# Kernel tuning notes

Hardware: AMD Instinct MI355X
Metric: run time of the kernel (lower is better)

Reference implementation:

```python
import jax, jax.numpy as jnp
import numpy as np


def _cell_centered_coords(H, W):
    # cell-centered unit grid: coordinate k -> (k + 0.5) / n, meshgrid over (h1, w1, h2, w2)
    h = (jnp.arange(H, dtype=jnp.float32) + 0.5) / H
    w = (jnp.arange(W, dtype=jnp.float32) + 0.5) / W
    g = jnp.meshgrid(h, w, h, w, indexing='ij')
    return jnp.stack(g, axis=-1)  # (H, W, H, W, 4)


def setup_inputs() -> dict:
    key = jax.random.key(0)
    ks = jax.random.split(key, 6)
    B, I, O, H, W, HID = 8, 16, 16, 28, 28, 64
    s1 = 1.0 / np.sqrt(4.0)
    s2 = 1.0 / np.sqrt(HID)
    return {
        'v': jax.random.normal(ks[0], (B, I, H, W), dtype=jnp.float32),
        'W1': jax.random.uniform(ks[1], (4, HID), jnp.float32, -s1, s1),
        'b1': jax.random.uniform(ks[2], (HID,), jnp.float32, -s1, s1),
        'W2': jax.random.uniform(ks[3], (HID, O * I), jnp.float32, -s2, s2),
        'b2': jax.random.uniform(ks[4], (O * I,), jnp.float32, -s2, s2),
        'bias': jax.random.uniform(ks[5], (O, 1, 1), jnp.float32, -1.0 / np.sqrt(I), 1.0 / np.sqrt(I)),
    }


def reference(v, W1, b1, W2, b2, bias):
    H, W = v.shape[-2], v.shape[-1]
    I = v.shape[-3]
    O = W2.shape[-1] // I
    coords = _cell_centered_coords(H, W)                      # (H,W,H,W,4)
    hidden = jax.nn.gelu(coords @ W1 + b1, approximate=False)  # (H,W,H,W,64)
    kernel = (hidden @ W2 + b2).reshape(H, W, H, W, O, I)      # (h1,w1,h2,w2,O,I)
    # midpoint-rule quadrature weights on the unit square: 1/(H*W) per cell
    quad = 1.0 / (H * W)
    # einsum 'h1 w1 h2 w2 o i, n i h1 w2 -> n o h2 w2' (w1 summed out of kernel alone)
    out = jnp.einsum('pqrsoi,nips->nors', kernel, quad * v)
    return out + bias
```

## Files before the change

kernel.cpp:

```cpp
#include <hip/hip_runtime.h>

#define Hn 28
#define PQ 784
#define NI 128

typedef __attribute__((ext_vector_type(8))) short short8v;
typedef __attribute__((ext_vector_type(4))) float float4v;

__device__ __forceinline__ short f2bf(float x) {
    union { float f; unsigned u; } a; a.f = x;
    unsigned r = a.u + 0x7FFF + ((a.u >> 16) & 1);
    return (short)(r >> 16);
}

__global__ __launch_bounds__(256) void prep_kernel(
    const float* __restrict__ v, const float* __restrict__ W2,
    short* __restrict__ vTb, short* __restrict__ W2b, float* __restrict__ Vsum)
{
    const int b = blockIdx.x;
    const int t = threadIdx.x;
    if (b == NI) {
        for (int e = t; e < 8192; e += 256) {
            const float2 f = ((const float2*)W2)[e];
            short2 h; h.x = f2bf(f.x); h.y = f2bf(f.y);
            ((short2*)W2b)[e] = h;
        }
        return;
    }
    const int ni = b;
    for (int e = t; e < PQ; e += 256) {
        const int p = e / Hn;
        const int s = e - p * Hn;
        vTb[s * (NI * 32) + ni * 32 + p] = f2bf(v[ni * PQ + e]);
    }
    if (t < Hn) {
        *(uint2*)(vTb + t * (NI * 32) + ni * 32 + 28) = make_uint2(0u, 0u);
    }
    if (t < Hn) {
        const int s = t;
        float acc = 0.0f;
        #pragma unroll
        for (int p = 0; p < Hn; ++p) acc += v[ni * PQ + p * Hn + s];
        Vsum[s * NI + ni] = acc;
    }
}

__global__ __launch_bounds__(256, 4) void fused_kernel(
    const short* __restrict__ vTb, const short* __restrict__ W2b,
    const float* __restrict__ Vsum,
    const float* __restrict__ W1, const float* __restrict__ b1,
    const float* __restrict__ b2, const float* __restrict__ bias,
    float* __restrict__ out)
{
    __shared__ short sV[NI * 40];
    __shared__ short sHt[64 * 40];
    __shared__ short sTa[8 * 1032];
    __shared__ float sRed[4 * 256];
    __shared__ float sVs[NI];

    const int t = threadIdx.x;
    const int rs = blockIdx.x;
    const int r = rs / Hn;
    const int s = rs - r * Hn;

    {
        const short* src = vTb + s * (NI * 32);
        #pragma unroll
        for (int j = 0; j < 2; ++j) {
            const int idx = t + 256 * j;
            const int ni = idx >> 2;
            const int ko = (idx & 3) * 8;
            *(short8v*)&sV[ni * 40 + ko] = *(const short8v*)(src + ni * 32 + ko);
        }
    }
    if (t < NI) sVs[t] = Vsum[s * NI + t];

    {
        const int c = t & 63;
        const int pg = t >> 6;
        const float w0 = W1[c];
        const float Wc = W1[64 + c];
        const float w2 = W1[128 + c];
        const float w3 = W1[192 + c];
        const float inv = 1.0f / 28.0f;
        const float base = ((r + 0.5f) * inv) * w2 + ((s + 0.5f) * inv) * w3
                         + b1[c] + 0.5f * Wc;
        const float w0i = inv * w0;
        const float W2c = Wc * Wc;
        const float c2 = 1.1651786f * W2c;
        const float c4 = 0.0145213f * (W2c * W2c);
        #pragma unroll
        for (int pi = 0; pi < 7; ++pi) {
            const int p = pg * 7 + pi;
            const float m  = fmaf((float)p + 0.5f, w0i, base);
            const float m2 = m * m;
            const float E  = __builtin_amdgcn_exp2f(m2 * -0.72134752f);
            const float az = fabsf(m) * 0.70710678f;
            const float tt = __builtin_amdgcn_rcpf(fmaf(0.3275911f, az, 1.0f));
            float poly = fmaf(tt, 1.061405429f, -1.453152027f);
            poly = fmaf(tt, poly, 1.421413741f);
            poly = fmaf(tt, poly, -0.284496736f);
            poly = fmaf(tt, poly, 0.254829592f);
            poly = poly * tt;
            float erfv = fmaf(-poly, E, 1.0f);
            erfv = (m < 0.0f) ? -erfv : erfv;
            const float g   = 0.5f * m * (1.0f + erfv);
            const float phi = 0.39894228f * E;
            const float p4  = fmaf(-m2, m2, fmaf(7.0f, m2, -4.0f));
            const float corr = phi * fmaf(c4, p4, c2 * (2.0f - m2));
            sHt[c * 40 + p] = f2bf(fmaf(28.0f, g, corr));
        }
        if (pg == 3) *(uint2*)&sHt[c * 40 + 28] = make_uint2(0u, 0u);
    }
    __syncthreads();

    const int w  = t >> 6;
    const int l  = t & 63;
    const int lm = l & 15;
    const int q  = l >> 4;
    const int k0 = q * 8;

    {
        short8v aF[2], bF[4];
        aF[0] = *(const short8v*)&sV[(32 * w + lm) * 40 + k0];
        aF[1] = *(const short8v*)&sV[(32 * w + 16 + lm) * 40 + k0];
        #pragma unroll
        for (int nt = 0; nt < 4; ++nt)
            bF[nt] = *(const short8v*)&sHt[(16 * nt + lm) * 40 + k0];

        float4v accD[2][4];
        #pragma unroll
        for (int mt = 0; mt < 2; ++mt)
            #pragma unroll
            for (int nt = 0; nt < 4; ++nt)
                accD[mt][nt] = __builtin_amdgcn_mfma_f32_16x16x32_bf16(
                    aF[mt], bF[nt], (float4v)(0.0f), 0, 0, 0);

        #pragma unroll
        for (int mt = 0; mt < 2; ++mt) {
            const int n8 = 2 * w + mt;
            #pragma unroll
            for (int nt = 0; nt < 4; ++nt) {
                const int c = 16 * nt + lm;
                #pragma unroll
                for (int reg = 0; reg < 4; ++reg) {
                    const int i = q * 4 + reg;
                    sTa[n8 * 1032 + c * 16 + i] = f2bf(accD[mt][nt][reg]);
                }
            }
        }
    }
    __syncthreads();

    float4v accO = (float4v)(0.0f);
    #pragma unroll
    for (int st = 0; st < 8; ++st) {
        const int kb = w * 256 + st * 32 + k0;
        const short8v a = *(const short8v*)&sTa[(lm & 7) * 1032 + kb];
        const int c  = kb >> 4;
        const int i0 = kb & 15;
        const short8v bfr = *(const short8v*)&W2b[c * 256 + lm * 16 + i0];
        accO = __builtin_amdgcn_mfma_f32_16x16x32_bf16(a, bfr, accO, 0, 0, 0);
    }
    #pragma unroll
    for (int reg = 0; reg < 4; ++reg) {
        const int m = q * 4 + reg;
        sRed[w * 256 + m * 16 + lm] = accO[reg];
    }
    __syncthreads();

    if (t < NI) {
        const int n8 = t >> 4;
        const int o  = t & 15;
        const int e  = n8 * 16 + o;
        const float tot = sRed[e] + sRed[256 + e] + sRed[512 + e] + sRed[768 + e];
        float bsum = 0.0f;
        #pragma unroll
        for (int i = 0; i < 16; ++i)
            bsum = fmaf(b2[o * 16 + i], sVs[n8 * 16 + i], bsum);
        out[(n8 * 16 + o) * PQ + rs] = (tot + 28.0f * bsum) * (1.0f / 784.0f) + bias[o];
    }
}

extern "C" void kernel_launch(void* const* d_in, const int* in_sizes, int n_in,
                              void* d_out, int out_size, void* d_ws, size_t ws_size,
                              hipStream_t stream) {
    const float* v    = (const float*)d_in[0];
    const float* W1   = (const float*)d_in[1];
    const float* b1   = (const float*)d_in[2];
    const float* W2   = (const float*)d_in[3];
    const float* b2   = (const float*)d_in[4];
    const float* bias = (const float*)d_in[5];
    float* out = (float*)d_out;

    char* ws = (char*)d_ws;
    short* vTb  = (short*)(ws);
    short* W2b  = (short*)(ws + 229376);
    float* Vsum = (float*)(ws + 262144);

    prep_kernel<<<NI + 1, 256, 0, stream>>>(v, W2, vTb, W2b, Vsum);
    fused_kernel<<<PQ, 256, 0, stream>>>(vTb, W2b, Vsum, W1, b1, b2, bias, out);
}
```

Measured before the change: 72.94 us.

## Fold prep kernel into fused kernel, converting v and W2 to bf16 in-block

Result: slower. 80.18 us (+9.9%).

```diff
diff --git a/kernel.cpp b/kernel.cpp
--- a/kernel.cpp
+++ b/kernel.cpp
@@ -5,6 +5,7 @@
 #define NI 128
 
 typedef __attribute__((ext_vector_type(8))) short short8v;
+typedef __attribute__((ext_vector_type(4))) short short4v;
 typedef __attribute__((ext_vector_type(4))) float float4v;
 
 __device__ __forceinline__ short f2bf(float x) {
@@ -13,42 +14,9 @@
     return (short)(r >> 16);
 }
 
-__global__ __launch_bounds__(256) void prep_kernel(
-    const float* __restrict__ v, const float* __restrict__ W2,
-    short* __restrict__ vTb, short* __restrict__ W2b, float* __restrict__ Vsum)
-{
-    const int b = blockIdx.x;
-    const int t = threadIdx.x;
-    if (b == NI) {
-        for (int e = t; e < 8192; e += 256) {
-            const float2 f = ((const float2*)W2)[e];
-            short2 h; h.x = f2bf(f.x); h.y = f2bf(f.y);
-            ((short2*)W2b)[e] = h;
-        }
-        return;
-    }
-    const int ni = b;
-    for (int e = t; e < PQ; e += 256) {
-        const int p = e / Hn;
-        const int s = e - p * Hn;
-        vTb[s * (NI * 32) + ni * 32 + p] = f2bf(v[ni * PQ + e]);
-    }
-    if (t < Hn) {
-        *(uint2*)(vTb + t * (NI * 32) + ni * 32 + 28) = make_uint2(0u, 0u);
-    }
-    if (t < Hn) {
-        const int s = t;
-        float acc = 0.0f;
-        #pragma unroll
-        for (int p = 0; p < Hn; ++p) acc += v[ni * PQ + p * Hn + s];
-        Vsum[s * NI + ni] = acc;
-    }
-}
-
 __global__ __launch_bounds__(256, 4) void fused_kernel(
-    const short* __restrict__ vTb, const short* __restrict__ W2b,
-    const float* __restrict__ Vsum,
-    const float* __restrict__ W1, const float* __restrict__ b1,
+    const float* __restrict__ v, const float* __restrict__ W1,
+    const float* __restrict__ b1, const float* __restrict__ W2,
     const float* __restrict__ b2, const float* __restrict__ bias,
     float* __restrict__ out)
 {
@@ -63,17 +31,13 @@
     const int r = rs / Hn;
     const int s = rs - r * Hn;
 
-    {
-        const short* src = vTb + s * (NI * 32);
-        #pragma unroll
-        for (int j = 0; j < 2; ++j) {
-            const int idx = t + 256 * j;
-            const int ni = idx >> 2;
-            const int ko = (idx & 3) * 8;
-            *(short8v*)&sV[ni * 40 + ko] = *(const short8v*)(src + ni * 32 + ko);
-        }
+    const int ni0 = t & 127;
+    const int p0 = t >> 7;
+    float vreg[14];
+    #pragma unroll
+    for (int j = 0; j < 14; ++j) {
+        vreg[j] = v[ni0 * PQ + (p0 + 2 * j) * Hn + s];
     }
-    if (t < NI) sVs[t] = Vsum[s * NI + t];
 
     {
         const int c = t & 63;
@@ -112,7 +76,20 @@
         }
         if (pg == 3) *(uint2*)&sHt[c * 40 + 28] = make_uint2(0u, 0u);
     }
+
+    {
+        float psum = 0.0f;
+        #pragma unroll
+        for (int j = 0; j < 14; ++j) {
+            psum += vreg[j];
+            sV[ni0 * 40 + (p0 + 2 * j)] = f2bf(vreg[j]);
+        }
+        sRed[t] = psum;
+        if (t < NI) *(uint2*)&sV[t * 40 + 28] = make_uint2(0u, 0u);
+    }
     __syncthreads();
+
+    if (t < NI) sVs[t] = sRed[t] + sRed[t + NI];
 
     const int w  = t >> 6;
     const int l  = t & 63;
@@ -142,11 +119,12 @@
             #pragma unroll
             for (int nt = 0; nt < 4; ++nt) {
                 const int c = 16 * nt + lm;
-                #pragma unroll
-                for (int reg = 0; reg < 4; ++reg) {
-                    const int i = q * 4 + reg;
-                    sTa[n8 * 1032 + c * 16 + i] = f2bf(accD[mt][nt][reg]);
-                }
+                short4v pk;
+                pk[0] = f2bf(accD[mt][nt][0]);
+                pk[1] = f2bf(accD[mt][nt][1]);
+                pk[2] = f2bf(accD[mt][nt][2]);
+                pk[3] = f2bf(accD[mt][nt][3]);
+                *(short4v*)&sTa[n8 * 1032 + c * 16 + 4 * q] = pk;
             }
         }
     }
@@ -159,9 +137,17 @@
         const short8v a = *(const short8v*)&sTa[(lm & 7) * 1032 + kb];
         const int c  = kb >> 4;
         const int i0 = kb & 15;
-        const short8v bfr = *(const short8v*)&W2b[c * 256 + lm * 16 + i0];
+        const float* wrow = &W2[c * 256 + lm * 16 + i0];
+        const float4 wf0 = *(const float4*)&wrow[0];
+        const float4 wf1 = *(const float4*)&wrow[4];
+        short8v bfr;
+        bfr[0] = f2bf(wf0.x); bfr[1] = f2bf(wf0.y);
+        bfr[2] = f2bf(wf0.z); bfr[3] = f2bf(wf0.w);
+        bfr[4] = f2bf(wf1.x); bfr[5] = f2bf(wf1.y);
+        bfr[6] = f2bf(wf1.z); bfr[7] = f2bf(wf1.w);
         accO = __builtin_amdgcn_mfma_f32_16x16x32_bf16(a, bfr, accO, 0, 0, 0);
     }
+    __syncthreads();
     #pragma unroll
     for (int reg = 0; reg < 4; ++reg) {
         const int m = q * 4 + reg;
@@ -193,11 +179,5 @@
     const float* bias = (const float*)d_in[5];
     float* out = (float*)d_out;
 
-    char* ws = (char*)d_ws;
-    short* vTb  = (short*)(ws);
-    short* W2b  = (short*)(ws + 229376);
-    float* Vsum = (float*)(ws + 262144);
-
-    prep_kernel<<<NI + 1, 256, 0, stream>>>(v, W2, vTb, W2b, Vsum);
-    fused_kernel<<<PQ, 256, 0, stream>>>(vTb, W2b, Vsum, W1, b1, b2, bias, out);
+    fused_kernel<<<PQ, 256, 0, stream>>>(v, W1, b1, W2, b2, bias, out);
 }
```
